# Performance work log

Hardware: AMD Instinct MI355X
Metric: run time of the kernel (lower is better)

Reference implementation:

```python
import jax, jax.numpy as jnp
import numpy as np

B, T, C, M = 64, 1024, 256, 1024  # note: broadcast in the torch source forces M == T


def setup_inputs() -> dict:
    key = jax.random.key(0)
    k = jax.random.split(key, 6)
    x = jax.random.normal(k[0], (B, T, C), jnp.float32)
    memory = 0.02 * jax.random.normal(k[1], (1, M, C), jnp.float32)  # nn.init.normal_(std=0.02)
    w1 = jax.random.normal(k[2], (2 * C, 4 * C), jnp.float32) / np.sqrt(2 * C)
    b1 = jnp.zeros((4 * C,), jnp.float32)
    w2 = jax.random.normal(k[3], (4 * C, C), jnp.float32) / np.sqrt(4 * C)
    b2 = jnp.zeros((C,), jnp.float32)
    return {"x": x, "memory": memory, "w1": w1, "b1": b1, "w2": w2, "b2": b2}


def reference(x, memory, w1, b1, w2, b2):
    # x: [B,T,C], memory: [1,M,C] (shared across batch, expanded lazily)
    mem = memory[0]                                        # [M,C]
    energy = jnp.einsum('btc,mc->btm', x, mem)             # cross-attn scores
    weights = jax.nn.softmax(energy, axis=-1)              # [B,T,M]
    retrieved = jnp.einsum('btm,mc->btc', weights, mem)    # [B,T,C]
    cat = jnp.concatenate([x, retrieved], axis=-1)         # [B,T,2C] (forward output)
    # gate MLP: Linear(2C,4C) -> SiLU -> Linear(4C,C) -> Sigmoid
    h = jax.nn.silu(jnp.einsum('btk,kf->btf', cat, w1) + b1)
    update_gate = jax.nn.sigmoid(jnp.einsum('btf,fc->btc', h, w2) + b2)  # [B,T,C], T==M
    # memory blend + batch-mean reduction (side-effect update in torch, detached)
    x_mean = jnp.mean(x, axis=1, keepdims=True)            # [B,1,C]
    new_mem = memory * (1.0 - update_gate) + x_mean * update_gate  # [B,M,C]
    new_memory = jnp.mean(new_mem, axis=0, keepdims=True)  # [1,M,C]
    return cat, new_memory
```

## Files before the change

kernel.cpp:

```cpp
#include <hip/hip_runtime.h>
#include <hip/hip_bf16.h>


#define BT 65536

typedef short bf16x8 __attribute__((ext_vector_type(8)));
typedef float f32x4 __attribute__((ext_vector_type(4)));

__device__ __forceinline__ unsigned short f2bf(float f) {
    unsigned x = __float_as_uint(f);
    unsigned r = (x + 0x7FFFu + ((x >> 16) & 1u)) >> 16;
    return (unsigned short)r;
}
__device__ __forceinline__ float bf2f(unsigned short u) {
    return __uint_as_float(((unsigned)u) << 16);
}

__device__ __forceinline__ void async16(const unsigned short* g, unsigned short* l) {
    __builtin_amdgcn_global_load_lds((const __attribute__((address_space(1))) unsigned int*)g,
                                     (__attribute__((address_space(3))) unsigned int*)l,
                                     16, 0, 0);
}


__global__ __launch_bounds__(256) void prep_x(const float* __restrict__ x,
                                              float* __restrict__ cat_out,
                                              unsigned short* __restrict__ cat_b) {
    long tid = (long)blockIdx.x * 256 + threadIdx.x;
    long i4 = tid * 4;
    long row = i4 >> 8;
    int c = (int)(i4 & 255);
    float4 v = *(const float4*)&x[i4];
    *(float4*)&cat_out[row * 512 + c] = v;
    ushort4 b4;
    b4.x = f2bf(v.x); b4.y = f2bf(v.y); b4.z = f2bf(v.z); b4.w = f2bf(v.w);
    *(ushort4*)&cat_b[row * 512 + c] = b4;
}

__global__ __launch_bounds__(256) void prep_mem(const float* __restrict__ mem,
                                                unsigned short* __restrict__ mem_b,
                                                unsigned short* __restrict__ memT_b) {
    int tid = blockIdx.x * 256 + threadIdx.x;
    mem_b[tid] = f2bf(mem[tid]);
    int c = tid >> 10, m = tid & 1023;
    memT_b[tid] = f2bf(mem[m * 256 + c]);
}

__global__ __launch_bounds__(256) void prep_w1(const float* __restrict__ w1,
                                               unsigned short* __restrict__ w1T) {
    int tid = blockIdx.x * 256 + threadIdx.x;
    int f = tid >> 9, k = tid & 511;
    w1T[tid] = f2bf(w1[k * 1024 + f]);
}

__global__ __launch_bounds__(256) void prep_w2(const float* __restrict__ w2,
                                               unsigned short* __restrict__ w2T) {
    int tid = blockIdx.x * 256 + threadIdx.x;
    int c = tid >> 10, k = tid & 1023;
    w2T[tid] = f2bf(w2[k * 256 + c]);
}

__global__ __launch_bounds__(256) void xmean_k(const float* __restrict__ x,
                                               float* __restrict__ xmean) {
    int b = blockIdx.x;
    int t0 = blockIdx.y * 64;
    int c = threadIdx.x;
    float s = 0.f;
    for (int t = 0; t < 64; t++)
        s += x[((long)(b * 1024 + t0 + t)) * 256 + c];
    atomicAdd(&xmean[b * 256 + c], s * (1.f / 1024.f));
}

template <int MODE>
__global__ __launch_bounds__(256) void gemm_bt(const unsigned short* __restrict__ A, long lda,
                                               const unsigned short* __restrict__ Bt, int K,
                                               float* __restrict__ outF,
                                               unsigned short* __restrict__ outB,
                                               const float* __restrict__ bias) {
    const int t = threadIdx.x;
    const int wave = t >> 6, lane = t & 63;
    const int waveM = wave >> 1, waveN = wave & 1;
    const int quad = lane >> 4, l16 = lane & 15;
    const long n0 = (long)blockIdx.x * 128;
    const long m0 = (long)blockIdx.y * 128;

    __shared__ unsigned short lA[128 * 32];
    __shared__ unsigned short lB[128 * 32];

    f32x4 acc[4][4] = {};

    const int sRow = wave * 16 + (lane >> 2);
    const int sC = (lane & 3) ^ ((sRow >> 1) & 3);
    const unsigned short* Ag0 = A + (m0 + sRow) * lda + sC * 8;
    const unsigned short* Ag1 = Ag0 + 64 * lda;
    const unsigned short* Bg0 = Bt + (n0 + sRow) * (long)K + sC * 8;
    const unsigned short* Bg1 = Bg0 + 64 * (long)K;
    unsigned short* lA0 = &lA[wave * 512];
    unsigned short* lA1 = &lA[2048 + wave * 512];
    unsigned short* lB0 = &lB[wave * 512];
    unsigned short* lB1 = &lB[2048 + wave * 512];

    const int sx = (l16 >> 1) & 3;
    int aoff[4], boff[4];
#pragma unroll
    for (int i = 0; i < 4; i++) {
        aoff[i] = (waveM * 64 + i * 16 + l16) * 32 + ((quad ^ sx) * 8);
        boff[i] = (waveN * 64 + i * 16 + l16) * 32 + ((quad ^ sx) * 8);
    }

    for (int k0 = 0; k0 < K; k0 += 32) {
        __syncthreads();
        async16(Ag0 + k0, lA0);
        async16(Ag1 + k0, lA1);
        async16(Bg0 + k0, lB0);
        async16(Bg1 + k0, lB1);
        __syncthreads();

        bf16x8 af[4], bfr[4];
#pragma unroll
        for (int i = 0; i < 4; i++) af[i] = *(const bf16x8*)&lA[aoff[i]];
#pragma unroll
        for (int j = 0; j < 4; j++) bfr[j] = *(const bf16x8*)&lB[boff[j]];
#pragma unroll
        for (int i = 0; i < 4; i++)
#pragma unroll
            for (int j = 0; j < 4; j++)
                acc[i][j] = __builtin_amdgcn_mfma_f32_16x16x32_bf16(af[i], bfr[j], acc[i][j], 0, 0, 0);
    }

#pragma unroll
    for (int i = 0; i < 4; i++) {
#pragma unroll
        for (int j = 0; j < 4; j++) {
            long col = n0 + waveN * 64 + j * 16 + l16;
            float bval = (MODE == 2 || MODE == 3) ? bias[col] : 0.f;
#pragma unroll
            for (int r = 0; r < 4; r++) {
                long row = m0 + waveM * 64 + i * 16 + quad * 4 + r;
                float v = acc[i][j][r];
                if (MODE == 0) {
                    outB[row * 1024 + col] = f2bf(v);
                } else if (MODE == 1) {
                    long o = row * 512 + 256 + col;
                    outF[o] = v;
                    outB[o] = f2bf(v);
                } else if (MODE == 2) {
                    float z = v + bval;
                    float s = 1.f / (1.f + __expf(-z));
                    outB[row * 1024 + col] = f2bf(z * s);
                } else {
                    float z = v + bval;
                    outF[row * 256 + col] = 1.f / (1.f + __expf(-z));
                }
            }
        }
    }
}

__global__ __launch_bounds__(256) void softmax_rows(unsigned short* __restrict__ P) {
    long row = (long)blockIdx.x * 4 + (threadIdx.x >> 6);
    int lane = threadIdx.x & 63;
    unsigned short* p = P + row * 1024 + lane * 16;
    uint4 u0 = *(const uint4*)p;
    uint4 u1 = *(const uint4*)(p + 8);
    const unsigned short* ua = (const unsigned short*)&u0;
    const unsigned short* ub = (const unsigned short*)&u1;
    float v[16];
#pragma unroll
    for (int i = 0; i < 8; i++) { v[i] = bf2f(ua[i]); v[i + 8] = bf2f(ub[i]); }
    float m = -1e30f;
#pragma unroll
    for (int i = 0; i < 16; i++) m = fmaxf(m, v[i]);
    for (int off = 32; off >= 1; off >>= 1) m = fmaxf(m, __shfl_xor(m, off));
    float s = 0.f;
#pragma unroll
    for (int i = 0; i < 16; i++) { v[i] = __expf(v[i] - m); s += v[i]; }
    for (int off = 32; off >= 1; off >>= 1) s += __shfl_xor(s, off);
    float inv = 1.f / s;
    unsigned short o[16];
#pragma unroll
    for (int i = 0; i < 16; i++) o[i] = f2bf(v[i] * inv);
    *(uint4*)p = *(uint4*)&o[0];
    *(uint4*)(p + 8) = *(uint4*)&o[8];
}

__global__ __launch_bounds__(256) void reduce_mem(const float* __restrict__ gate,
                                                  const float* __restrict__ memory,
                                                  const float* __restrict__ xmean,
                                                  float* __restrict__ out2) {
    int m = blockIdx.x, c = threadIdx.x;
    float mm = memory[m * 256 + c];
    float s = 0.f;
    for (int b = 0; b < 64; b++)
        s += gate[((long)(b * 1024 + m)) * 256 + c] * (xmean[b * 256 + c] - mm);
    out2[m * 256 + c] = mm + s * (1.f / 64.f);
}

extern "C" void kernel_launch(void* const* d_in, const int* in_sizes, int n_in,
                              void* d_out, int out_size, void* d_ws, size_t ws_size,
                              hipStream_t stream) {
    const float* x      = (const float*)d_in[0];
    const float* memory = (const float*)d_in[1];
    const float* w1     = (const float*)d_in[2];
    const float* b1     = (const float*)d_in[3];
    const float* w2     = (const float*)d_in[4];
    const float* b2     = (const float*)d_in[5];
    float* out = (float*)d_out;

    unsigned short* mem_b  = (unsigned short*)d_ws;
    unsigned short* memT_b = mem_b + 262144;
    unsigned short* w1T    = memT_b + 262144;
    unsigned short* w2T    = w1T + 524288;
    float* xmean           = (float*)(w2T + 262144);
    unsigned short* cat_b  = (unsigned short*)(xmean + 16384);
    unsigned short* Pbuf   = cat_b + 33554432;
    float* gate            = (float*)cat_b;

    hipMemsetAsync(xmean, 0, 64 * 256 * sizeof(float), stream);

    prep_mem<<<1024, 256, 0, stream>>>(memory, mem_b, memT_b);
    prep_w1<<<2048, 256, 0, stream>>>(w1, w1T);
    prep_w2<<<1024, 256, 0, stream>>>(w2, w2T);
    prep_x<<<16384, 256, 0, stream>>>(x, out, cat_b);
    xmean_k<<<dim3(64, 16), 256, 0, stream>>>(x, xmean);

    gemm_bt<0><<<dim3(8, 512), 256, 0, stream>>>(cat_b, 512, mem_b, 256, nullptr, Pbuf, nullptr);
    softmax_rows<<<16384, 256, 0, stream>>>(Pbuf);
    gemm_bt<1><<<dim3(2, 512), 256, 0, stream>>>(Pbuf, 1024, memT_b, 1024, out, cat_b, nullptr);
    gemm_bt<2><<<dim3(8, 512), 256, 0, stream>>>(cat_b, 512, w1T, 512, nullptr, Pbuf, b1);
    gemm_bt<3><<<dim3(2, 512), 256, 0, stream>>>(Pbuf, 1024, w2T, 1024, gate, nullptr, b2);

    reduce_mem<<<1024, 256, 0, stream>>>(gate, memory, xmean, out + 33554432);
}
```

Measured before the change: 619.4 us.

## Double-buffer LDS tiles in bf16 GEMM and swizzle workgroup-to-tile mapping

Converts the GEMM main loop to double-buffered LDS, issuing the async global-to-LDS loads for the next K-slice before computing the current one. This is meant to overlap memory latency with MFMA work and to drop one barrier per iteration. Workgroup IDs are also remapped with a stride-8 swizzle so that concurrently running blocks, which may sit on different XCDs, share tiles in cache. The cost is twice the LDS footprint, which may reduce occupancy, and the swizzle assumes the workgroup count is divisible by 8.

Measured after the change: 579.2 us. -6.5%, faster.

```diff
diff --git a/kernel.cpp b/kernel.cpp
--- a/kernel.cpp
+++ b/kernel.cpp
@@ -71,6 +71,23 @@
     atomicAdd(&xmean[b * 256 + c], s * (1.f / 1024.f));
 }
 
+
+__device__ __forceinline__ void compute_tile(const unsigned short* bufA,
+                                             const unsigned short* bufB,
+                                             const int* aoff, const int* boff,
+                                             f32x4 acc[4][4]) {
+    bf16x8 af[4], bfr[4];
+#pragma unroll
+    for (int i = 0; i < 4; i++) af[i] = *(const bf16x8*)&bufA[aoff[i]];
+#pragma unroll
+    for (int j = 0; j < 4; j++) bfr[j] = *(const bf16x8*)&bufB[boff[j]];
+#pragma unroll
+    for (int i = 0; i < 4; i++)
+#pragma unroll
+        for (int j = 0; j < 4; j++)
+            acc[i][j] = __builtin_amdgcn_mfma_f32_16x16x32_bf16(af[i], bfr[j], acc[i][j], 0, 0, 0);
+}
+
 template <int MODE>
 __global__ __launch_bounds__(256) void gemm_bt(const unsigned short* __restrict__ A, long lda,
                                                const unsigned short* __restrict__ Bt, int K,
@@ -81,11 +98,17 @@
     const int wave = t >> 6, lane = t & 63;
     const int waveM = wave >> 1, waveN = wave & 1;
     const int quad = lane >> 4, l16 = lane & 15;
-    const long n0 = (long)blockIdx.x * 128;
-    const long m0 = (long)blockIdx.y * 128;
-
-    __shared__ unsigned short lA[128 * 32];
-    __shared__ unsigned short lB[128 * 32];
+
+    const int nwg = gridDim.x * gridDim.y;
+    const int lid = blockIdx.y * gridDim.x + blockIdx.x;
+    const int sid = (lid & 7) * (nwg >> 3) + (lid >> 3);
+    const int nb = sid % gridDim.x;
+    const int mb = sid / gridDim.x;
+    const long n0 = (long)nb * 128;
+    const long m0 = (long)mb * 128;
+
+    __shared__ unsigned short lA[2][128 * 32];
+    __shared__ unsigned short lB[2][128 * 32];
 
     f32x4 acc[4][4] = {};
 
@@ -95,10 +118,8 @@
     const unsigned short* Ag1 = Ag0 + 64 * lda;
     const unsigned short* Bg0 = Bt + (n0 + sRow) * (long)K + sC * 8;
     const unsigned short* Bg1 = Bg0 + 64 * (long)K;
-    unsigned short* lA0 = &lA[wave * 512];
-    unsigned short* lA1 = &lA[2048 + wave * 512];
-    unsigned short* lB0 = &lB[wave * 512];
-    unsigned short* lB1 = &lB[2048 + wave * 512];
+    const int so0 = wave * 512;
+    const int so1 = 2048 + wave * 512;
 
     const int sx = (l16 >> 1) & 3;
     int aoff[4], boff[4];
@@ -108,25 +129,34 @@
         boff[i] = (waveN * 64 + i * 16 + l16) * 32 + ((quad ^ sx) * 8);
     }
 
-    for (int k0 = 0; k0 < K; k0 += 32) {
-        __syncthreads();
-        async16(Ag0 + k0, lA0);
-        async16(Ag1 + k0, lA1);
-        async16(Bg0 + k0, lB0);
-        async16(Bg1 + k0, lB1);
-        __syncthreads();
-
-        bf16x8 af[4], bfr[4];
-#pragma unroll
-        for (int i = 0; i < 4; i++) af[i] = *(const bf16x8*)&lA[aoff[i]];
-#pragma unroll
-        for (int j = 0; j < 4; j++) bfr[j] = *(const bf16x8*)&lB[boff[j]];
-#pragma unroll
-        for (int i = 0; i < 4; i++)
-#pragma unroll
-            for (int j = 0; j < 4; j++)
-                acc[i][j] = __builtin_amdgcn_mfma_f32_16x16x32_bf16(af[i], bfr[j], acc[i][j], 0, 0, 0);
+#define STAGE(BUF, KOFF) do {                       \
+        async16(Ag0 + (KOFF), &lA[BUF][so0]);       \
+        async16(Ag1 + (KOFF), &lA[BUF][so1]);       \
+        async16(Bg0 + (KOFF), &lB[BUF][so0]);       \
+        async16(Bg1 + (KOFF), &lB[BUF][so1]);       \
+    } while (0)
+
+#define WAITBAR() do {                                      \
+        asm volatile("s_waitcnt vmcnt(0)" ::: "memory");    \
+        __builtin_amdgcn_s_barrier();                       \
+        __builtin_amdgcn_sched_barrier(0);                  \
+    } while (0)
+
+    const int nk = K >> 5;
+    STAGE(0, 0);
+    WAITBAR();
+
+    int cur = 0;
+    for (int kt = 0; kt < nk - 1; ++kt) {
+        STAGE(cur ^ 1, (kt + 1) << 5);
+        compute_tile(&lA[cur][0], &lB[cur][0], aoff, boff, acc);
+        WAITBAR();
+        cur ^= 1;
     }
+    compute_tile(&lA[cur][0], &lB[cur][0], aoff, boff, acc);
+
+#undef STAGE
+#undef WAITBAR
 
 #pragma unroll
     for (int i = 0; i < 4; i++) {
```

## Restructure GEMM: stage 256-wide B chunks in LDS, load A directly, remap workgroups

Applied to the files above, without the earlier changes.

The GEMM kernel now stages a 128x256 slice of B in LDS per chunk instead of 32-wide K tiles, so it synchronises once per chunk rather than on every K step. A fragments are read straight from global memory into registers, and register double-buffering prefetches the next k-step's fragments while the MFMAs run. Workgroup IDs are remapped in groups of eight, and K and lda become template constants so the loops fully unroll. The cost is 64KB of LDS per block, which lowers occupancy, and uncached direct global reads of A that may be less coalesced.

Measured after the change: 706.8 us. +14.1%, slower.

```diff
diff --git a/kernel.cpp b/kernel.cpp
--- a/kernel.cpp
+++ b/kernel.cpp
@@ -71,62 +71,94 @@
     atomicAdd(&xmean[b * 256 + c], s * (1.f / 1024.f));
 }
 
-template <int MODE>
-__global__ __launch_bounds__(256) void gemm_bt(const unsigned short* __restrict__ A, long lda,
-                                               const unsigned short* __restrict__ Bt, int K,
+template <int MODE, int K>
+__global__ __launch_bounds__(256) void gemm_bt(const unsigned short* __restrict__ A,
+                                               const unsigned short* __restrict__ Bt,
                                                float* __restrict__ outF,
                                                unsigned short* __restrict__ outB,
                                                const float* __restrict__ bias) {
+    constexpr int LDA = (MODE == 0 || MODE == 2) ? 512 : 1024;
+    constexpr int NC = K / 256;
     const int t = threadIdx.x;
     const int wave = t >> 6, lane = t & 63;
     const int waveM = wave >> 1, waveN = wave & 1;
     const int quad = lane >> 4, l16 = lane & 15;
-    const long n0 = (long)blockIdx.x * 128;
-    const long m0 = (long)blockIdx.y * 128;
-
-    __shared__ unsigned short lA[128 * 32];
-    __shared__ unsigned short lB[128 * 32];
+
+    const int nwg = gridDim.x * gridDim.y;
+    const int lid = blockIdx.y * gridDim.x + blockIdx.x;
+    const int sid = (lid & 7) * (nwg >> 3) + (lid >> 3);
+    const int nb = sid % gridDim.x;
+    const int mb = sid / gridDim.x;
+    const long n0 = (long)nb * 128;
+    const long m0 = (long)mb * 128;
+
+    __shared__ unsigned short lB[128 * 256];
 
     f32x4 acc[4][4] = {};
 
-    const int sRow = wave * 16 + (lane >> 2);
-    const int sC = (lane & 3) ^ ((sRow >> 1) & 3);
-    const unsigned short* Ag0 = A + (m0 + sRow) * lda + sC * 8;
-    const unsigned short* Ag1 = Ag0 + 64 * lda;
-    const unsigned short* Bg0 = Bt + (n0 + sRow) * (long)K + sC * 8;
-    const unsigned short* Bg1 = Bg0 + 64 * (long)K;
-    unsigned short* lA0 = &lA[wave * 512];
-    unsigned short* lA1 = &lA[2048 + wave * 512];
-    unsigned short* lB0 = &lB[wave * 512];
-    unsigned short* lB1 = &lB[2048 + wave * 512];
-
-    const int sx = (l16 >> 1) & 3;
-    int aoff[4], boff[4];
-#pragma unroll
-    for (int i = 0; i < 4; i++) {
-        aoff[i] = (waveM * 64 + i * 16 + l16) * 32 + ((quad ^ sx) * 8);
-        boff[i] = (waveN * 64 + i * 16 + l16) * 32 + ((quad ^ sx) * 8);
+    const int rw = wave * 2 + (lane >> 5);
+    const int sc = lane & 31;
+    const unsigned short* Bg = Bt + (n0 + rw) * (long)K + (long)((sc ^ rw) * 8);
+
+#define STAGE_B(CH) do {                                                   \
+        _Pragma("unroll")                                                  \
+        for (int j = 0; j < 16; j++)                                       \
+            async16(Bg + (long)j * (8 * K) + (CH) * 256,                   \
+                    &lB[j * 2048 + wave * 512]);                           \
+    } while (0)
+
+    const unsigned short* Ap[4];
+#pragma unroll
+    for (int i = 0; i < 4; i++)
+        Ap[i] = A + (m0 + waveM * 64 + i * 16 + l16) * (long)LDA + quad * 8;
+
+    const int bx = l16 & 7;
+    int brow[4];
+#pragma unroll
+    for (int j = 0; j < 4; j++)
+        brow[j] = (waveN * 64 + j * 16 + l16) * 256;
+
+    STAGE_B(0);
+    asm volatile("s_waitcnt vmcnt(0)" ::: "memory");
+    __builtin_amdgcn_s_barrier();
+    __builtin_amdgcn_sched_barrier(0);
+
+#pragma unroll
+    for (int c = 0; c < NC; ++c) {
+        const int kb = c * 256;
+        bf16x8 af[2][4], bfr[2][4];
+#pragma unroll
+        for (int i = 0; i < 4; i++) af[0][i] = *(const bf16x8*)(Ap[i] + kb);
+#pragma unroll
+        for (int j = 0; j < 4; j++) bfr[0][j] = *(const bf16x8*)&lB[brow[j] + ((quad ^ bx) * 8)];
+#pragma unroll
+        for (int kk = 0; kk < 8; ++kk) {
+            const int cur = kk & 1, nxt = cur ^ 1;
+            if (kk < 7) {
+#pragma unroll
+                for (int i = 0; i < 4; i++)
+                    af[nxt][i] = *(const bf16x8*)(Ap[i] + kb + (kk + 1) * 32);
+#pragma unroll
+                for (int j = 0; j < 4; j++)
+                    bfr[nxt][j] = *(const bf16x8*)&lB[brow[j] + ((((kk + 1) * 4 + quad) ^ bx) * 8)];
+            }
+#pragma unroll
+            for (int i = 0; i < 4; i++)
+#pragma unroll
+                for (int j = 0; j < 4; j++)
+                    acc[i][j] = __builtin_amdgcn_mfma_f32_16x16x32_bf16(af[cur][i], bfr[cur][j], acc[i][j], 0, 0, 0);
+        }
+        if (c + 1 < NC) {
+            asm volatile("s_waitcnt lgkmcnt(0)" ::: "memory");
+            __builtin_amdgcn_sched_barrier(0);
+            __builtin_amdgcn_s_barrier();
+            STAGE_B(c + 1);
+            asm volatile("s_waitcnt vmcnt(0)" ::: "memory");
+            __builtin_amdgcn_s_barrier();
+            __builtin_amdgcn_sched_barrier(0);
+        }
     }
-
-    for (int k0 = 0; k0 < K; k0 += 32) {
-        __syncthreads();
-        async16(Ag0 + k0, lA0);
-        async16(Ag1 + k0, lA1);
-        async16(Bg0 + k0, lB0);
-        async16(Bg1 + k0, lB1);
-        __syncthreads();
-
-        bf16x8 af[4], bfr[4];
-#pragma unroll
-        for (int i = 0; i < 4; i++) af[i] = *(const bf16x8*)&lA[aoff[i]];
-#pragma unroll
-        for (int j = 0; j < 4; j++) bfr[j] = *(const bf16x8*)&lB[boff[j]];
-#pragma unroll
-        for (int i = 0; i < 4; i++)
-#pragma unroll
-            for (int j = 0; j < 4; j++)
-                acc[i][j] = __builtin_amdgcn_mfma_f32_16x16x32_bf16(af[i], bfr[j], acc[i][j], 0, 0, 0);
-    }
+#undef STAGE_B
 
 #pragma unroll
     for (int i = 0; i < 4; i++) {
@@ -224,11 +256,11 @@
     prep_x<<<16384, 256, 0, stream>>>(x, out, cat_b);
     xmean_k<<<dim3(64, 16), 256, 0, stream>>>(x, xmean);
 
-    gemm_bt<0><<<dim3(8, 512), 256, 0, stream>>>(cat_b, 512, mem_b, 256, nullptr, Pbuf, nullptr);
+    gemm_bt<0, 256><<<dim3(8, 512), 256, 0, stream>>>(cat_b, mem_b, nullptr, Pbuf, nullptr);
     softmax_rows<<<16384, 256, 0, stream>>>(Pbuf);
-    gemm_bt<1><<<dim3(2, 512), 256, 0, stream>>>(Pbuf, 1024, memT_b, 1024, out, cat_b, nullptr);
-    gemm_bt<2><<<dim3(8, 512), 256, 0, stream>>>(cat_b, 512, w1T, 512, nullptr, Pbuf, b1);
-    gemm_bt<3><<<dim3(2, 512), 256, 0, stream>>>(Pbuf, 1024, w2T, 1024, gate, nullptr, b2);
+    gemm_bt<1, 1024><<<dim3(2, 512), 256, 0, stream>>>(Pbuf, memT_b, out, cat_b, nullptr);
+    gemm_bt<2, 512><<<dim3(8, 512), 256, 0, stream>>>(cat_b, w1T, nullptr, Pbuf, b1);
+    gemm_bt<3, 1024><<<dim3(2, 512), 256, 0, stream>>>(Pbuf, w2T, gate, nullptr, b2);
 
     reduce_mem<<<1024, 256, 0, stream>>>(gate, memory, xmean, out + 33554432);
 }
```

## Rewrite bf16 GEMM with 256x256 tiles, double-buffered async LDS pipeline, and XCD swizzle

Applied to the files above, without the earlier changes.

Replaces the 128x128, single-buffered GEMM (two barriers per 32-wide K step) with a 512-thread kernel computing 256x256 tiles. The new kernel stages 64-wide K slices into double-buffered LDS with async global-to-LDS loads and overlaps the loads with MFMA phases using explicit waitcnt, setprio and sched_barrier. It also remaps block IDs so neighbouring tiles group together across XCDs, and makes K a compile-time constant. The aim is to hide memory latency and raise MFMA utilisation, at the cost of more LDS (128 KB) and more registers, which limits occupancy.

After: 605.6 us. 1.02x faster.

```diff
diff --git a/kernel.cpp b/kernel.cpp
--- a/kernel.cpp
+++ b/kernel.cpp
@@ -20,6 +20,10 @@
     __builtin_amdgcn_global_load_lds((const __attribute__((address_space(1))) unsigned int*)g,
                                      (__attribute__((address_space(3))) unsigned int*)l,
                                      16, 0, 0);
+}
+
+__device__ __forceinline__ f32x4 mfma16(bf16x8 a, bf16x8 b, f32x4 c) {
+    return __builtin_amdgcn_mfma_f32_16x16x32_bf16(a, b, c, 0, 0, 0);
 }
 
 
@@ -71,73 +75,133 @@
     atomicAdd(&xmean[b * 256 + c], s * (1.f / 1024.f));
 }
 
-template <int MODE>
-__global__ __launch_bounds__(256) void gemm_bt(const unsigned short* __restrict__ A, long lda,
-                                               const unsigned short* __restrict__ Bt, int K,
-                                               float* __restrict__ outF,
-                                               unsigned short* __restrict__ outB,
-                                               const float* __restrict__ bias) {
+template <int MODE, int K>
+__global__ __launch_bounds__(512, 2) void gemm_bt(const unsigned short* __restrict__ A,
+                                                  const unsigned short* __restrict__ Bt,
+                                                  float* __restrict__ outF,
+                                                  unsigned short* __restrict__ outB,
+                                                  const float* __restrict__ bias) {
+    constexpr long LDA = (MODE == 0 || MODE == 2) ? 512 : 1024;
+    constexpr int NX = (MODE == 0 || MODE == 2) ? 4 : 1;
+    constexpr int NWG = NX * 256;
+    constexpr int NT = K / 64;
+
     const int t = threadIdx.x;
     const int wave = t >> 6, lane = t & 63;
-    const int waveM = wave >> 1, waveN = wave & 1;
+    const int waveM = wave >> 2, waveN = wave & 3;
     const int quad = lane >> 4, l16 = lane & 15;
-    const long n0 = (long)blockIdx.x * 128;
-    const long m0 = (long)blockIdx.y * 128;
-
-    __shared__ unsigned short lA[128 * 32];
-    __shared__ unsigned short lB[128 * 32];
-
-    f32x4 acc[4][4] = {};
-
-    const int sRow = wave * 16 + (lane >> 2);
-    const int sC = (lane & 3) ^ ((sRow >> 1) & 3);
-    const unsigned short* Ag0 = A + (m0 + sRow) * lda + sC * 8;
-    const unsigned short* Ag1 = Ag0 + 64 * lda;
-    const unsigned short* Bg0 = Bt + (n0 + sRow) * (long)K + sC * 8;
-    const unsigned short* Bg1 = Bg0 + 64 * (long)K;
-    unsigned short* lA0 = &lA[wave * 512];
-    unsigned short* lA1 = &lA[2048 + wave * 512];
-    unsigned short* lB0 = &lB[wave * 512];
-    unsigned short* lB1 = &lB[2048 + wave * 512];
-
-    const int sx = (l16 >> 1) & 3;
-    int aoff[4], boff[4];
-#pragma unroll
-    for (int i = 0; i < 4; i++) {
-        aoff[i] = (waveM * 64 + i * 16 + l16) * 32 + ((quad ^ sx) * 8);
-        boff[i] = (waveN * 64 + i * 16 + l16) * 32 + ((quad ^ sx) * 8);
+
+    const int lid = blockIdx.y * NX + blockIdx.x;
+    const int sid = (lid & 7) * (NWG >> 3) + (lid >> 3);
+    const int nb = sid % NX;
+    const int mb = sid / NX;
+    const long n0 = (long)nb * 256;
+    const long m0 = (long)mb * 256;
+
+    __shared__ unsigned short lA[2][256 * 64];
+    __shared__ unsigned short lB[2][256 * 64];
+
+    f32x4 acc[8][4] = {};
+    bf16x8 aW[4][2], bAll[4][2];
+
+    const int srow = t >> 3;
+    const int schk = (t & 7) ^ (srow & 7);
+    const unsigned short* aS = A + (m0 + srow) * LDA + schk * 8;
+    const unsigned short* bS = Bt + (n0 + srow) * (long)K + schk * 8;
+
+#define STAGE_A(BUF, KT) do { _Pragma("unroll")                               \
+        for (int c = 0; c < 4; c++)                                           \
+            async16(aS + (long)c * 64 * LDA + (KT) * 64,                      \
+                    &lA[BUF][(c * 64 + wave * 8) * 64]); } while (0)
+#define STAGE_B(BUF, KT) do { _Pragma("unroll")                               \
+        for (int c = 0; c < 4; c++)                                           \
+            async16(bS + (long)c * 64 * (long)K + (KT) * 64,                  \
+                    &lB[BUF][(c * 64 + wave * 8) * 64]); } while (0)
+
+    const int sx = l16 & 7;
+    const int aBase = (waveM * 128 + l16) * 64;
+    const int bBase = (waveN * 64 + l16) * 64;
+    const int c0 = ((quad    ) ^ sx) * 8;
+    const int c1 = ((quad + 4) ^ sx) * 8;
+
+#define RD_A(BUF, MLO) do { _Pragma("unroll")                                 \
+        for (int m = 0; m < 4; m++) {                                         \
+            aW[m][0] = *(const bf16x8*)&lA[BUF][aBase + ((MLO) + m) * 1024 + c0]; \
+            aW[m][1] = *(const bf16x8*)&lA[BUF][aBase + ((MLO) + m) * 1024 + c1]; \
+        } } while (0)
+#define RD_B(BUF, NLO) do { _Pragma("unroll")                                 \
+        for (int n = 0; n < 2; n++) {                                         \
+            bAll[(NLO) + n][0] = *(const bf16x8*)&lB[BUF][bBase + ((NLO) + n) * 1024 + c0]; \
+            bAll[(NLO) + n][1] = *(const bf16x8*)&lB[BUF][bBase + ((NLO) + n) * 1024 + c1]; \
+        } } while (0)
+#define MM(MLO, NLO) do { _Pragma("unroll")                                   \
+        for (int m = 0; m < 4; m++) { _Pragma("unroll")                       \
+            for (int n = 0; n < 2; n++) {                                     \
+                acc[(MLO)+m][(NLO)+n] = mfma16(aW[m][0], bAll[(NLO)+n][0], acc[(MLO)+m][(NLO)+n]); \
+                acc[(MLO)+m][(NLO)+n] = mfma16(aW[m][1], bAll[(NLO)+n][1], acc[(MLO)+m][(NLO)+n]); \
+            } } } while (0)
+
+#define PH_IN()  do { __builtin_amdgcn_sched_barrier(0);                      \
+        __builtin_amdgcn_s_barrier();                                         \
+        asm volatile("s_waitcnt lgkmcnt(0)" ::: "memory");                    \
+        __builtin_amdgcn_sched_barrier(0);                                    \
+        __builtin_amdgcn_s_setprio(1); } while (0)
+#define PH_OUT() do { __builtin_amdgcn_s_setprio(0);                          \
+        __builtin_amdgcn_sched_barrier(0);                                    \
+        __builtin_amdgcn_s_barrier(); } while (0)
+
+#define GROUP(KT, BUF, DOSTAGE, DOWAIT0) do {                                 \
+                                                                     \
+        RD_A(BUF, 0); RD_B(BUF, 0);                                           \
+        PH_IN(); MM(0, 0); PH_OUT();                                          \
+                                                                     \
+        RD_B(BUF, 2);                                                         \
+        PH_IN(); MM(0, 2); PH_OUT();                                          \
+                                                                     \
+        RD_A(BUF, 4);                                                         \
+        if (DOSTAGE) STAGE_B(BUF, (KT) + 2);                                  \
+        PH_IN(); MM(4, 0); PH_OUT();                                          \
+                                                                     \
+        if (DOSTAGE) {                                                        \
+            STAGE_A(BUF, (KT) + 2);                                           \
+            asm volatile("s_waitcnt vmcnt(8)" ::: "memory");                  \
+        } else if (DOWAIT0) {                                                 \
+            asm volatile("s_waitcnt vmcnt(0)" ::: "memory");                  \
+        }                                                                     \
+        PH_IN(); MM(4, 2); PH_OUT();                                          \
+    } while (0)
+
+    STAGE_A(0, 0); STAGE_B(0, 0);
+    STAGE_A(1, 1); STAGE_B(1, 1);
+    asm volatile("s_waitcnt vmcnt(8)" ::: "memory");
+    __builtin_amdgcn_s_barrier();
+    __builtin_amdgcn_sched_barrier(0);
+
+#pragma unroll 1
+    for (int kt = 0; kt < NT; kt += 2) {
+        GROUP(kt, 0, kt + 2 < NT, kt + 1 < NT);
+        GROUP(kt + 1, 1, kt + 3 < NT, kt + 2 < NT);
     }
 
-    for (int k0 = 0; k0 < K; k0 += 32) {
-        __syncthreads();
-        async16(Ag0 + k0, lA0);
-        async16(Ag1 + k0, lA1);
-        async16(Bg0 + k0, lB0);
-        async16(Bg1 + k0, lB1);
-        __syncthreads();
-
-        bf16x8 af[4], bfr[4];
-#pragma unroll
-        for (int i = 0; i < 4; i++) af[i] = *(const bf16x8*)&lA[aoff[i]];
-#pragma unroll
-        for (int j = 0; j < 4; j++) bfr[j] = *(const bf16x8*)&lB[boff[j]];
-#pragma unroll
-        for (int i = 0; i < 4; i++)
-#pragma unroll
-            for (int j = 0; j < 4; j++)
-                acc[i][j] = __builtin_amdgcn_mfma_f32_16x16x32_bf16(af[i], bfr[j], acc[i][j], 0, 0, 0);
-    }
-
-#pragma unroll
-    for (int i = 0; i < 4; i++) {
-#pragma unroll
-        for (int j = 0; j < 4; j++) {
-            long col = n0 + waveN * 64 + j * 16 + l16;
-            float bval = (MODE == 2 || MODE == 3) ? bias[col] : 0.f;
+#undef GROUP
+#undef PH_IN
+#undef PH_OUT
+#undef MM
+#undef RD_A
+#undef RD_B
+#undef STAGE_A
+#undef STAGE_B
+
+#pragma unroll
+    for (int n = 0; n < 4; n++) {
+        long col = n0 + waveN * 64 + n * 16 + l16;
+        float bval = (MODE == 2 || MODE == 3) ? bias[col] : 0.f;
+#pragma unroll
+        for (int m = 0; m < 8; m++) {
 #pragma unroll
             for (int r = 0; r < 4; r++) {
-                long row = m0 + waveM * 64 + i * 16 + quad * 4 + r;
-                float v = acc[i][j][r];
+                long row = m0 + waveM * 128 + m * 16 + quad * 4 + r;
+                float v = acc[m][n][r];
                 if (MODE == 0) {
                     outB[row * 1024 + col] = f2bf(v);
                 } else if (MODE == 1) {
@@ -224,11 +288,11 @@
     prep_x<<<16384, 256, 0, stream>>>(x, out, cat_b);
     xmean_k<<<dim3(64, 16), 256, 0, stream>>>(x, xmean);
 
-    gemm_bt<0><<<dim3(8, 512), 256, 0, stream>>>(cat_b, 512, mem_b, 256, nullptr, Pbuf, nullptr);
+    gemm_bt<0, 256><<<dim3(4, 256), 512, 0, stream>>>(cat_b, mem_b, nullptr, Pbuf, nullptr);
     softmax_rows<<<16384, 256, 0, stream>>>(Pbuf);
-    gemm_bt<1><<<dim3(2, 512), 256, 0, stream>>>(Pbuf, 1024, memT_b, 1024, out, cat_b, nullptr);
-    gemm_bt<2><<<dim3(8, 512), 256, 0, stream>>>(cat_b, 512, w1T, 512, nullptr, Pbuf, b1);
-    gemm_bt<3><<<dim3(2, 512), 256, 0, stream>>>(Pbuf, 1024, w2T, 1024, gate, nullptr, b2);
+    gemm_bt<1, 1024><<<dim3(1, 256), 512, 0, stream>>>(Pbuf, memT_b, out, cat_b, nullptr);
+    gemm_bt<2, 512><<<dim3(4, 256), 512, 0, stream>>>(cat_b, w1T, nullptr, Pbuf, b1);
+    gemm_bt<3, 1024><<<dim3(1, 256), 512, 0, stream>>>(Pbuf, w2T, gate, nullptr, b2);
 
     reduce_mem<<<1024, 256, 0, stream>>>(gate, memory, xmean, out + 33554432);
 }
```
